# Kernel tuning notes

Measured on AMD Instinct MI355X. Metric: run time of the kernel, lower is better.

The kernel has to match this reference:

```python
import jax, jax.numpy as jnp
import numpy as np

N, G, NPG, K = 65536, 64, 1024, 32
NB, BD, IN_CH, GNN_DIM, L = 64, 4, 256, 256, 2
NBP = (BD - 1) * BD // 2 * NB  # 384
E = 524288


def setup_inputs():
    key = jax.random.key(0)
    ks = jax.random.split(key, 10)
    s = 0.05
    return {
        "x": jax.random.normal(ks[0], (N, IN_CH), jnp.float32),
        "eigvec": jax.random.normal(ks[1], (N, K), jnp.float32) / np.float32(np.sqrt(NPG)),
        "eigval": jax.random.uniform(ks[2], (G, K), jnp.float32, 0.0, 2.0),
        "taus": jnp.ones((NB,), jnp.float32),
        "enc_w": jax.random.normal(ks[3], (IN_CH, GNN_DIM), jnp.float32) * s,
        "enc_b": jnp.zeros((GNN_DIM,), jnp.float32),
        "self_w": jax.random.normal(ks[4], (L, GNN_DIM, GNN_DIM), jnp.float32) * s,
        "self_b": jnp.zeros((L, GNN_DIM), jnp.float32),
        "nb_w": jax.random.normal(ks[5], (L, GNN_DIM, GNN_DIM), jnp.float32) * s,
        "nb_b": jnp.zeros((L, GNN_DIM), jnp.float32),
        "dec_w": jax.random.normal(ks[6], (GNN_DIM, NBP), jnp.float32) * s,
        "dec_b": jnp.zeros((NBP,), jnp.float32),
        "lin_w": jax.random.normal(ks[7], (IN_CH, IN_CH), jnp.float32) * s,
        "lin_b": jnp.zeros((IN_CH,), jnp.float32),
        "edge_index": jax.random.randint(ks[8], (2, E), 0, N, jnp.int32),
    }


def _householder(p):
    # p: [M, BD*(BD-1)//2] -> Q: [M, BD, BD], product of BD-1 Householder reflectors
    M = p.shape[0]
    Q = jnp.broadcast_to(jnp.eye(BD, dtype=p.dtype), (M, BD, BD))
    idx = 0
    for j in range(BD - 1):  # small fixed loop over bundle_dim-1 reflectors
        n = BD - 1 - j
        v = jnp.zeros((M, BD), p.dtype).at[:, j].set(1.0)
        v = v.at[:, j + 1:].set(p[:, idx:idx + n])
        idx += n
        nrm = jnp.sum(v * v, axis=1)[:, None, None]
        Qv = jnp.einsum('mij,mj->mi', Q, v)
        Q = Q - 2.0 * Qv[:, :, None] * v[:, None, :] / nrm
    return Q


def reference(x, eigvec, eigval, taus, enc_w, enc_b, self_w, self_b,
              nb_w, nb_b, dec_w, dec_b, lin_w, lin_b, edge_index):
    gelu = lambda t: jax.nn.gelu(t, approximate=False)
    src, dst = edge_index[0], edge_index[1]
    vf = x.reshape(N, NB, BD, -1)                      # [N, NB, BD, 1]
    # SumGNN structural encoder: h = gelu(enc(x)); residual GNN layers; dec
    h = gelu(x @ enc_w + enc_b)
    for k in range(L):
        agg = jax.ops.segment_sum(h[src], dst, num_segments=N)  # sum aggregation
        hk = (h @ self_w[k] + self_b[k]) + (agg @ nb_w[k] + nb_b[k])
        h = gelu(hk) + h
    node_rep = h @ dec_w + dec_b                       # [N, NBP]
    Q = _householder(node_rep.reshape(N * NB, NBP // NB)).reshape(N, NB, BD, BD)
    vf = jnp.einsum('abcd,abde->abce', Q, vf)          # bundle transform
    h = vf.reshape(G, NPG, IN_CH)                      # to_dense_batch (equal-size graphs)
    ev = eigvec.reshape(G, NPG, K)
    hs = jnp.einsum('gnv,gnd->gvd', ev, h)             # project onto eigenbasis
    fact = jnp.exp(-eigval[:, :, None] * taus[None, None, :])   # [G, K, NB]
    hs = (hs.reshape(G, K, NB, BD, -1) * fact[..., None, None]).reshape(G, K, IN_CH)
    h = jnp.einsum('gnv,gvd->gnd', ev, hs).reshape(N, IN_CH)     # reproject
    h = h @ lin_w + lin_b
    vf = jnp.einsum('abdc,abde->abce', Q, h.reshape(N, NB, BD, -1))  # Q^T
    return vf.reshape(N, IN_CH)
```

## Files before the change

### kernel.cpp

```cpp
#include <hip/hip_runtime.h>
#include <math.h>

#define NN      65536
#define GG      64
#define NPG     1024
#define KEIG    32
#define NBUN    64
#define BDIM    4
#define CH      256
#define NBP     384
#define NEDGE   524288

using f16x8 = __attribute__((ext_vector_type(8))) _Float16;
using f16x4 = __attribute__((ext_vector_type(4))) _Float16;
using f32x4 = __attribute__((ext_vector_type(4))) float;

__device__ __forceinline__ float gelu_f(float x) {
    return 0.5f * x * (1.0f + erff(x * 0.70710678118654752440f));
}

template<int NOUT, int KTOT, bool DUAL, bool ACT, bool RESA, bool WF, bool W16>
__global__ __launch_bounds__(NOUT, 2) void mgemm_k(
    const _Float16* __restrict__ A1, const _Float16* __restrict__ A2,
    const _Float16* __restrict__ Bp, const float* __restrict__ bias,
    float* __restrict__ Cf, _Float16* __restrict__ C16)
{
    constexpr int NT   = KTOT / 32;
    constexpr int ROWB = KTOT * 2;
    constexpr int CPR  = KTOT / 8;
    __shared__ _Float16 Alds[64 * KTOT];

    const int tid  = threadIdx.x;
    const int lane = tid & 63;
    const int wave = tid >> 6;
    const int m0   = blockIdx.x * 64;

    constexpr int TOTC = 64 * CPR;
    constexpr int NSTG = TOTC / NOUT;
    {
        f16x8 stg[NSTG ? NSTG : 1];
#pragma unroll
        for (int j = 0; j < NSTG; j++) {
            const int idx = tid + j * NOUT;
            const int r = idx / CPR, c = idx - r * CPR;
            const _Float16* src = (DUAL && c >= CPR / 2)
                ? A2 + (size_t)(m0 + r) * 256 + (c - CPR / 2) * 8
                : A1 + (size_t)(m0 + r) * 256 + c * 8;
            stg[j] = *(const f16x8*)src;
        }
#pragma unroll
        for (int j = 0; j < NSTG; j++) {
            const int idx = tid + j * NOUT;
            const int r = idx / CPR, c = idx - r * CPR;
            *(f16x8*)((char*)Alds + ((r * ROWB + c * 16) ^ ((r & 7) << 4))) = stg[j];
        }
        if (TOTC % NOUT) {
            const int idx = tid + NSTG * NOUT;
            if (idx < TOTC) {
                const int r = idx / CPR, c = idx - r * CPR;
                const _Float16* src = (DUAL && c >= CPR / 2)
                    ? A2 + (size_t)(m0 + r) * 256 + (c - CPR / 2) * 8
                    : A1 + (size_t)(m0 + r) * 256 + c * 8;
                f16x8 v = *(const f16x8*)src;
                *(f16x8*)((char*)Alds + ((r * ROWB + c * 16) ^ ((r & 7) << 4))) = v;
            }
        }
    }
    __syncthreads();

    const int r16 = lane & 15;
    const int kc  = lane >> 4;

    const _Float16* bpp = Bp + ((size_t)wave * NT * 2048) + lane * 8;

    f32x4 acc[4][4];
#pragma unroll
    for (int i = 0; i < 4; i++)
#pragma unroll
        for (int j = 0; j < 4; j++) acc[i][j] = 0.f;

    f16x8 p00, p01, p02, p03, p10, p11, p12, p13;

#define LDB(P0, P1, P2, P3, T)                                                 \
    {                                                                          \
        const _Float16* bq_ = bpp + (size_t)(T) * 2048;                        \
        P0 = *(const f16x8*)(bq_);                                             \
        P1 = *(const f16x8*)(bq_ + 512);                                       \
        P2 = *(const f16x8*)(bq_ + 1024);                                      \
        P3 = *(const f16x8*)(bq_ + 1536);                                      \
    }

#define MSTEP(OFF, P0, P1, P2, P3)                                             \
    {                                                                          \
        const char* ap_ = (const char*)Alds + (OFF);                           \
        f16x8 a0_ = *(const f16x8*)(ap_);                                      \
        f16x8 a1_ = *(const f16x8*)(ap_ + 16 * ROWB);                          \
        f16x8 a2_ = *(const f16x8*)(ap_ + 32 * ROWB);                          \
        f16x8 a3_ = *(const f16x8*)(ap_ + 48 * ROWB);                          \
        acc[0][0] = __builtin_amdgcn_mfma_f32_16x16x32_f16(a0_, P0, acc[0][0], 0, 0, 0); \
        acc[0][1] = __builtin_amdgcn_mfma_f32_16x16x32_f16(a0_, P1, acc[0][1], 0, 0, 0); \
        acc[0][2] = __builtin_amdgcn_mfma_f32_16x16x32_f16(a0_, P2, acc[0][2], 0, 0, 0); \
        acc[0][3] = __builtin_amdgcn_mfma_f32_16x16x32_f16(a0_, P3, acc[0][3], 0, 0, 0); \
        acc[1][0] = __builtin_amdgcn_mfma_f32_16x16x32_f16(a1_, P0, acc[1][0], 0, 0, 0); \
        acc[1][1] = __builtin_amdgcn_mfma_f32_16x16x32_f16(a1_, P1, acc[1][1], 0, 0, 0); \
        acc[1][2] = __builtin_amdgcn_mfma_f32_16x16x32_f16(a1_, P2, acc[1][2], 0, 0, 0); \
        acc[1][3] = __builtin_amdgcn_mfma_f32_16x16x32_f16(a1_, P3, acc[1][3], 0, 0, 0); \
        acc[2][0] = __builtin_amdgcn_mfma_f32_16x16x32_f16(a2_, P0, acc[2][0], 0, 0, 0); \
        acc[2][1] = __builtin_amdgcn_mfma_f32_16x16x32_f16(a2_, P1, acc[2][1], 0, 0, 0); \
        acc[2][2] = __builtin_amdgcn_mfma_f32_16x16x32_f16(a2_, P2, acc[2][2], 0, 0, 0); \
        acc[2][3] = __builtin_amdgcn_mfma_f32_16x16x32_f16(a2_, P3, acc[2][3], 0, 0, 0); \
        acc[3][0] = __builtin_amdgcn_mfma_f32_16x16x32_f16(a3_, P0, acc[3][0], 0, 0, 0); \
        acc[3][1] = __builtin_amdgcn_mfma_f32_16x16x32_f16(a3_, P1, acc[3][1], 0, 0, 0); \
        acc[3][2] = __builtin_amdgcn_mfma_f32_16x16x32_f16(a3_, P2, acc[3][2], 0, 0, 0); \
        acc[3][3] = __builtin_amdgcn_mfma_f32_16x16x32_f16(a3_, P3, acc[3][3], 0, 0, 0); \
    }

    LDB(p00, p01, p02, p03, 0)
    LDB(p10, p11, p12, p13, 1)

    int au = r16 * ROWB + kc * 16;
    const int swz = (r16 & 7) << 4;
    for (int t = 0; t < NT; t += 2) {
        MSTEP(au ^ swz, p00, p01, p02, p03)
        if (t + 2 < NT) LDB(p00, p01, p02, p03, t + 2)
        MSTEP((au + 64) ^ swz, p10, p11, p12, p13)
        if (t + 3 < NT) LDB(p10, p11, p12, p13, t + 3)
        au += 128;
    }
#undef LDB
#undef MSTEP

    const int rbase = (lane >> 4) * 4;
    const int ncol  = lane & 15;
#pragma unroll
    for (int nt = 0; nt < 4; nt++) {
        const int n = wave * 64 + nt * 16 + ncol;
        const float bs = bias[n];
#pragma unroll
        for (int mt = 0; mt < 4; mt++) {
#pragma unroll
            for (int i = 0; i < 4; i++) {
                const int m = m0 + mt * 16 + rbase + i;
                const size_t idx = (size_t)m * NOUT + n;
                float v = acc[mt][nt][i] + bs;
                if (ACT) v = gelu_f(v);
                if (RESA) v += (float)A1[(size_t)m * 256 + n];
                if (WF) Cf[idx] = v;
                if (W16) C16[idx] = (_Float16)v;
            }
        }
    }
}

template<int NOUT, int KTOT, bool DUAL>
__global__ __launch_bounds__(256) void pack_k(
    const float* __restrict__ W1, const float* __restrict__ W2,
    _Float16* __restrict__ Bp)
{
    constexpr int NT = KTOT / 32;
    const int cid = blockIdx.x * 256 + threadIdx.x;
    if (cid >= NOUT * KTOT / 8) return;
    const int l  = cid & 63;
    const int q  = (cid >> 6) & 3;
    const int c2 = cid >> 8;
    const int t  = c2 & (NT - 1);
    const int wn = c2 / NT;
    const int n  = wn * 64 + q * 16 + (l & 15);
    const int k0 = t * 32 + (l >> 4) * 8;
    f16x8 v;
#pragma unroll
    for (int j = 0; j < 8; j++) {
        const int k = k0 + j;
        float w = (DUAL && k >= 256) ? W2[(size_t)(k - 256) * NOUT + n]
                                     : W1[(size_t)k * NOUT + n];
        v[j] = (_Float16)w;
    }
    *(f16x8*)(Bp + (size_t)cid * 8) = v;
}

__global__ void zero_k(float* __restrict__ p, size_t n)
{
    size_t i = (size_t)blockIdx.x * blockDim.x + threadIdx.x;
    float4* p4 = (float4*)p;
    size_t n4 = n >> 2;
    for (size_t j = i; j < n4; j += (size_t)gridDim.x * blockDim.x)
        p4[j] = make_float4(0.f, 0.f, 0.f, 0.f);
}

__global__ __launch_bounds__(256) void cvt16_k(
    const float* __restrict__ in, _Float16* __restrict__ out)
{
    size_t i = (size_t)blockIdx.x * 256 + threadIdx.x;
    float4 v = ((const float4*)in)[i];
    f16x4 o = { (_Float16)v.x, (_Float16)v.y, (_Float16)v.z, (_Float16)v.w };
    ((f16x4*)out)[i] = o;
}

__global__ void bcomb_k(const float* __restrict__ a, const float* __restrict__ b,
                        float* __restrict__ o)
{
    int i = blockIdx.x * 256 + threadIdx.x;
    if (i < 512) o[i] = a[i] + b[i];
}

__global__ __launch_bounds__(256) void hist_k(const int* __restrict__ ei, int* __restrict__ deg)
{
    int e = blockIdx.x * 256 + threadIdx.x;
    if (e < NEDGE) atomicAdd(&deg[ei[NEDGE + e]], 1);
}

__global__ __launch_bounds__(1024) void scan_k(
    const int* __restrict__ deg, int* __restrict__ off, int* __restrict__ cursor)
{
    __shared__ int sh[1024];
    const int tid = threadIdx.x;
    const int base = tid * 64;
    int s = 0;
#pragma unroll 8
    for (int i = 0; i < 64; i++) s += deg[base + i];
    const int mysum = s;
    sh[tid] = s;
    __syncthreads();
    for (int ofs = 1; ofs < 1024; ofs <<= 1) {
        int v = (tid >= ofs) ? sh[tid - ofs] : 0;
        __syncthreads();
        sh[tid] += v;
        __syncthreads();
    }
    int running = sh[tid] - mysum;
    for (int i = 0; i < 64; i++) {
        off[base + i] = running;
        cursor[base + i] = running;
        running += deg[base + i];
    }
    if (tid == 1023) off[NN] = running;
}

__global__ __launch_bounds__(256) void fill_k(
    const int* __restrict__ ei, int* __restrict__ cursor, int* __restrict__ csr)
{
    int e = blockIdx.x * 256 + threadIdx.x;
    if (e < NEDGE) {
        int d = ei[NEDGE + e];
        int pos = atomicAdd(&cursor[d], 1);
        csr[pos] = ei[e];
    }
}

__global__ __launch_bounds__(256) void gather16_k(
    const _Float16* __restrict__ h, const int* __restrict__ off,
    const int* __restrict__ csr, _Float16* __restrict__ agg)
{
    const int lane = threadIdx.x & 63;
    const int n = blockIdx.x * 4 + (threadIdx.x >> 6);
    const int s0 = off[n], s1 = off[n + 1];
    float a0 = 0.f, a1 = 0.f, a2 = 0.f, a3 = 0.f;
    int j = s0;
    for (; j + 1 < s1; j += 2) {
        f16x4 va = ((const f16x4*)(h + (size_t)csr[j] * CH))[lane];
        f16x4 vb = ((const f16x4*)(h + (size_t)csr[j + 1] * CH))[lane];
        a0 += (float)va[0] + (float)vb[0]; a1 += (float)va[1] + (float)vb[1];
        a2 += (float)va[2] + (float)vb[2]; a3 += (float)va[3] + (float)vb[3];
    }
    if (j < s1) {
        f16x4 va = ((const f16x4*)(h + (size_t)csr[j] * CH))[lane];
        a0 += (float)va[0]; a1 += (float)va[1]; a2 += (float)va[2]; a3 += (float)va[3];
    }
    f16x4 o = { (_Float16)a0, (_Float16)a1, (_Float16)a2, (_Float16)a3 };
    ((f16x4*)(agg + (size_t)n * CH))[lane] = o;
}

__device__ __forceinline__ void make_Q(const _Float16* __restrict__ p, float Q[4][4])
{
#pragma unroll
    for (int i = 0; i < 4; i++)
#pragma unroll
        for (int j = 0; j < 4; j++) Q[i][j] = (i == j) ? 1.f : 0.f;
    int idx = 0;
#pragma unroll
    for (int j = 0; j < 3; j++) {
        float v[4] = {0.f, 0.f, 0.f, 0.f};
        v[j] = 1.f;
#pragma unroll
        for (int t = 0; t < 4; t++)
            if (t > j) v[t] = (float)p[idx + t - (j + 1)];
        idx += 3 - j;
        float nrm = v[0]*v[0] + v[1]*v[1] + v[2]*v[2] + v[3]*v[3];
        float s = 2.f / nrm;
#pragma unroll
        for (int i = 0; i < 4; i++) {
            float qv = Q[i][0]*v[0] + Q[i][1]*v[1] + Q[i][2]*v[2] + Q[i][3]*v[3];
            float t0 = s * qv;
#pragma unroll
            for (int c = 0; c < 4; c++) Q[i][c] -= t0 * v[c];
        }
    }
}

template<bool TRANS>
__global__ __launch_bounds__(256) void bundle_k(
    const float* __restrict__ vin, const _Float16* __restrict__ nr,
    float* __restrict__ out)
{
    __shared__ _Float16 pb[4 * NBP];
    const int n0 = blockIdx.x * 4;
    for (int i = threadIdx.x; i < 4 * NBP; i += 256)
        pb[i] = nr[(size_t)n0 * NBP + i];
    __syncthreads();
    const int ln = threadIdx.x >> 6;
    const int b  = threadIdx.x & 63;
    const int n  = n0 + ln;
    float Q[4][4];
    make_Q(&pb[ln * NBP + b * 6], Q);
    float4 xv = ((const float4*)(vin + (size_t)n * CH))[b];
    float in0 = xv.x, in1 = xv.y, in2 = xv.z, in3 = xv.w;
    float4 o;
    if constexpr (!TRANS) {
        o.x = Q[0][0]*in0 + Q[0][1]*in1 + Q[0][2]*in2 + Q[0][3]*in3;
        o.y = Q[1][0]*in0 + Q[1][1]*in1 + Q[1][2]*in2 + Q[1][3]*in3;
        o.z = Q[2][0]*in0 + Q[2][1]*in1 + Q[2][2]*in2 + Q[2][3]*in3;
        o.w = Q[3][0]*in0 + Q[3][1]*in1 + Q[3][2]*in2 + Q[3][3]*in3;
    } else {
        o.x = Q[0][0]*in0 + Q[1][0]*in1 + Q[2][0]*in2 + Q[3][0]*in3;
        o.y = Q[0][1]*in0 + Q[1][1]*in1 + Q[2][1]*in2 + Q[3][1]*in3;
        o.z = Q[0][2]*in0 + Q[1][2]*in1 + Q[2][2]*in2 + Q[3][2]*in3;
        o.w = Q[0][3]*in0 + Q[1][3]*in1 + Q[2][3]*in2 + Q[3][3]*in3;
    }
    ((float4*)(out + (size_t)n * CH))[b] = o;
}

__global__ __launch_bounds__(256) void spec_proj_k(
    const float* __restrict__ v, const float* __restrict__ eigvec, float* __restrict__ hs)
{
    const int g = blockIdx.x;
    const int nbase = g * NPG + blockIdx.y * 128;
    __shared__ float evs[16][32];
    float acc[32];
#pragma unroll
    for (int k = 0; k < 32; k++) acc[k] = 0.f;
    for (int nt = 0; nt < 128; nt += 16) {
        __syncthreads();
        for (int i = threadIdx.x; i < 512; i += 256) {
            int nn = i >> 5, kk = i & 31;
            evs[nn][kk] = eigvec[(size_t)(nbase + nt + nn) * KEIG + kk];
        }
        __syncthreads();
#pragma unroll 4
        for (int nn = 0; nn < 16; nn++) {
            float hv = v[(size_t)(nbase + nt + nn) * CH + threadIdx.x];
#pragma unroll
            for (int k = 0; k < 32; k++) acc[k] += evs[nn][k] * hv;
        }
    }
    float* o = hs + (size_t)g * KEIG * CH + threadIdx.x;
#pragma unroll
    for (int k = 0; k < 32; k++) atomicAdd(o + k * CH, acc[k]);
}

__global__ __launch_bounds__(256) void spec_reproj16_k(
    const float* __restrict__ eigvec, const float* __restrict__ hs,
    const float* __restrict__ eigval, const float* __restrict__ taus,
    _Float16* __restrict__ out16)
{
    const int g = blockIdx.x >> 4;
    const int nbase = g * NPG + (blockIdx.x & 15) * 64;
    const float tau = taus[threadIdx.x >> 2];
    float hsr[32];
    const float* hg = hs + (size_t)g * KEIG * CH + threadIdx.x;
#pragma unroll
    for (int k = 0; k < 32; k++)
        hsr[k] = hg[k * CH] * expf(-eigval[g * KEIG + k] * tau);
    __shared__ float evs[64][32];
    for (int i = threadIdx.x; i < 2048; i += 256) {
        int nn = i >> 5, kk = i & 31;
        evs[nn][kk] = eigvec[(size_t)(nbase + nn) * KEIG + kk];
    }
    __syncthreads();
    for (int nn = 0; nn < 64; nn++) {
        float a = 0.f;
#pragma unroll
        for (int k = 0; k < 32; k++) a += evs[nn][k] * hsr[k];
        out16[(size_t)(nbase + nn) * CH + threadIdx.x] = (_Float16)a;
    }
}

extern "C" void kernel_launch(void* const* d_in, const int* in_sizes, int n_in,
                              void* d_out, int out_size, void* d_ws, size_t ws_size,
                              hipStream_t stream)
{
    const float* x      = (const float*)d_in[0];
    const float* eigvec = (const float*)d_in[1];
    const float* eigval = (const float*)d_in[2];
    const float* taus   = (const float*)d_in[3];
    const float* enc_w  = (const float*)d_in[4];
    const float* enc_b  = (const float*)d_in[5];
    const float* self_w = (const float*)d_in[6];
    const float* self_b = (const float*)d_in[7];
    const float* nb_w   = (const float*)d_in[8];
    const float* nb_b   = (const float*)d_in[9];
    const float* dec_w  = (const float*)d_in[10];
    const float* dec_b  = (const float*)d_in[11];
    const float* lin_w  = (const float*)d_in[12];
    const float* lin_b  = (const float*)d_in[13];
    const int*   ei     = (const int*)d_in[14];
    (void)in_sizes; (void)n_in; (void)out_size; (void)ws_size;

    float* ws = (float*)d_ws;
    _Float16* x16 = (_Float16*)(ws);
    _Float16* h0  = (_Float16*)(ws + 8388608);
    _Float16* h1  = (_Float16*)(ws + 16777216);
    _Float16* agg = (_Float16*)(ws + 25165824);
    int* ibase  = (int*)(ws + 33554432);
    int* deg    = ibase;
    int* off    = ibase + 65536;
    int* cursor = ibase + 131073;
    int* csr    = ibase + 196609;
    _Float16* nr16 = (_Float16*)(ws + 25165824);
    float* wb = ws + 37748752;
    _Float16* enc16 = (_Float16*)(wb);
    _Float16* l1w   = (_Float16*)(wb + 32768);
    _Float16* l2w   = (_Float16*)(wb + 98304);
    _Float16* dec16 = (_Float16*)(wb + 163840);
    _Float16* lin16 = (_Float16*)(wb + 212992);
    float* lbias = wb + 245760;
    _Float16* h2 = (_Float16*)(ws + 37995024);
    float* vf1 = ws;
    float* hs  = ws + 16777216;
    float* h3  = vf1;

    dim3 blk(256);

    cvt16_k<<<16384, blk, 0, stream>>>(x, x16);
    pack_k<256, 256, false><<<32, blk, 0, stream>>>(enc_w, nullptr, enc16);
    pack_k<256, 512, true ><<<64, blk, 0, stream>>>(self_w,         nb_w,         l1w);
    pack_k<256, 512, true ><<<64, blk, 0, stream>>>(self_w + 65536, nb_w + 65536, l2w);
    pack_k<384, 256, false><<<48, blk, 0, stream>>>(dec_w, nullptr, dec16);
    pack_k<256, 256, false><<<32, blk, 0, stream>>>(lin_w, nullptr, lin16);
    bcomb_k<<<2, blk, 0, stream>>>(self_b, nb_b, lbias);
    zero_k<<<64, blk, 0, stream>>>((float*)deg, (size_t)NN);
    hist_k<<<NEDGE / 256, blk, 0, stream>>>(ei, deg);
    scan_k<<<1, 1024, 0, stream>>>(deg, off, cursor);
    fill_k<<<NEDGE / 256, blk, 0, stream>>>(ei, cursor, csr);

    mgemm_k<256, 256, false, true, false, false, true><<<dim3(1024), blk, 0, stream>>>(
        x16, nullptr, enc16, enc_b, nullptr, h0);

    gather16_k<<<NN / 4, blk, 0, stream>>>(h0, off, csr, agg);
    mgemm_k<256, 512, true, true, true, false, true><<<dim3(1024), blk, 0, stream>>>(
        h0, agg, l1w, lbias, nullptr, h1);

    gather16_k<<<NN / 4, blk, 0, stream>>>(h1, off, csr, agg);
    mgemm_k<256, 512, true, true, true, false, true><<<dim3(1024), blk, 0, stream>>>(
        h1, agg, l2w, lbias + 256, nullptr, h0);

    mgemm_k<384, 256, false, false, false, false, true><<<dim3(1024), dim3(384), 0, stream>>>(
        h0, nullptr, dec16, dec_b, nullptr, nr16);

    bundle_k<false><<<NN / 4, blk, 0, stream>>>(x, nr16, vf1);

    zero_k<<<512, blk, 0, stream>>>(hs, (size_t)GG * KEIG * CH);
    spec_proj_k<<<dim3(GG, 8), blk, 0, stream>>>(vf1, eigvec, hs);
    spec_reproj16_k<<<GG * 16, blk, 0, stream>>>(eigvec, hs, eigval, taus, h2);

    mgemm_k<256, 256, false, false, false, true, false><<<dim3(1024), blk, 0, stream>>>(
        h2, nullptr, lin16, lin_b, h3, nullptr);

    bundle_k<true><<<NN / 4, blk, 0, stream>>>(h3, nr16, (float*)d_out);
}
```

Measured before the change: 711.5 us.

## Deepen B prefetch, stage fp16 epilogue through LDS, unroll gather by four

The GEMM kernel now issues B-fragment loads for four k-steps before the A tile is staged, so global B latency overlaps the LDS fill. The main loop uses a four-deep register ring and is fully unrolled. The fp16 output path writes results into a padded LDS tile and stores them as coalesced 16-byte rows instead of scattered 2-byte writes. The edge gather loop is unrolled by four to raise memory-level parallelism. In exchange, register pressure rises, which may lower occupancy under the launch bound of 2, and two extra barriers are added in the epilogue.

```diff
diff --git a/kernel.cpp b/kernel.cpp
--- a/kernel.cpp
+++ b/kernel.cpp
@@ -28,12 +28,38 @@
     constexpr int NT   = KTOT / 32;
     constexpr int ROWB = KTOT * 2;
     constexpr int CPR  = KTOT / 8;
-    __shared__ _Float16 Alds[64 * KTOT];
+    constexpr int CTS  = NOUT + 8;
+    constexpr int AH   = 64 * KTOT;
+    constexpr int CTH  = 64 * CTS;
+    constexpr int LDSH = (W16 && CTH > AH) ? CTH : AH;
+    __shared__ _Float16 Alds[LDSH];
 
     const int tid  = threadIdx.x;
     const int lane = tid & 63;
     const int wave = tid >> 6;
     const int m0   = blockIdx.x * 64;
+
+    const int r16 = lane & 15;
+    const int kc  = lane >> 4;
+
+    const _Float16* bpp = Bp + ((size_t)wave * NT * 2048) + lane * 8;
+
+    f16x8 pa0, pa1, pa2, pa3, pb0, pb1, pb2, pb3;
+    f16x8 pc0, pc1, pc2, pc3, pd0, pd1, pd2, pd3;
+
+#define LDB(P0, P1, P2, P3, T)                                                 \
+    {                                                                          \
+        const _Float16* bq_ = bpp + (size_t)(T) * 2048;                        \
+        P0 = *(const f16x8*)(bq_);                                             \
+        P1 = *(const f16x8*)(bq_ + 512);                                       \
+        P2 = *(const f16x8*)(bq_ + 1024);                                      \
+        P3 = *(const f16x8*)(bq_ + 1536);                                      \
+    }
+
+    LDB(pa0, pa1, pa2, pa3, 0)
+    LDB(pb0, pb1, pb2, pb3, 1)
+    LDB(pc0, pc1, pc2, pc3, 2)
+    LDB(pd0, pd1, pd2, pd3, 3)
 
     constexpr int TOTC = 64 * CPR;
     constexpr int NSTG = TOTC / NOUT;
@@ -68,27 +94,11 @@
     }
     __syncthreads();
 
-    const int r16 = lane & 15;
-    const int kc  = lane >> 4;
-
-    const _Float16* bpp = Bp + ((size_t)wave * NT * 2048) + lane * 8;
-
     f32x4 acc[4][4];
 #pragma unroll
     for (int i = 0; i < 4; i++)
 #pragma unroll
         for (int j = 0; j < 4; j++) acc[i][j] = 0.f;
-
-    f16x8 p00, p01, p02, p03, p10, p11, p12, p13;
-
-#define LDB(P0, P1, P2, P3, T)                                                 \
-    {                                                                          \
-        const _Float16* bq_ = bpp + (size_t)(T) * 2048;                        \
-        P0 = *(const f16x8*)(bq_);                                             \
-        P1 = *(const f16x8*)(bq_ + 512);                                       \
-        P2 = *(const f16x8*)(bq_ + 1024);                                      \
-        P3 = *(const f16x8*)(bq_ + 1536);                                      \
-    }
 
 #define MSTEP(OFF, P0, P1, P2, P3)                                             \
     {                                                                          \
@@ -115,38 +125,68 @@
         acc[3][3] = __builtin_amdgcn_mfma_f32_16x16x32_f16(a3_, P3, acc[3][3], 0, 0, 0); \
     }
 
-    LDB(p00, p01, p02, p03, 0)
-    LDB(p10, p11, p12, p13, 1)
-
     int au = r16 * ROWB + kc * 16;
     const int swz = (r16 & 7) << 4;
-    for (int t = 0; t < NT; t += 2) {
-        MSTEP(au ^ swz, p00, p01, p02, p03)
-        if (t + 2 < NT) LDB(p00, p01, p02, p03, t + 2)
-        MSTEP((au + 64) ^ swz, p10, p11, p12, p13)
-        if (t + 3 < NT) LDB(p10, p11, p12, p13, t + 3)
-        au += 128;
+#pragma unroll
+    for (int t = 0; t < NT; t += 4) {
+        MSTEP((au      ) ^ swz, pa0, pa1, pa2, pa3)
+        if (t + 4 < NT) LDB(pa0, pa1, pa2, pa3, t + 4)
+        MSTEP((au +  64) ^ swz, pb0, pb1, pb2, pb3)
+        if (t + 5 < NT) LDB(pb0, pb1, pb2, pb3, t + 5)
+        MSTEP((au + 128) ^ swz, pc0, pc1, pc2, pc3)
+        if (t + 6 < NT) LDB(pc0, pc1, pc2, pc3, t + 6)
+        MSTEP((au + 192) ^ swz, pd0, pd1, pd2, pd3)
+        if (t + 7 < NT) LDB(pd0, pd1, pd2, pd3, t + 7)
+        au += 256;
     }
 #undef LDB
 #undef MSTEP
 
     const int rbase = (lane >> 4) * 4;
     const int ncol  = lane & 15;
-#pragma unroll
-    for (int nt = 0; nt < 4; nt++) {
-        const int n = wave * 64 + nt * 16 + ncol;
-        const float bs = bias[n];
-#pragma unroll
-        for (int mt = 0; mt < 4; mt++) {
-#pragma unroll
-            for (int i = 0; i < 4; i++) {
-                const int m = m0 + mt * 16 + rbase + i;
-                const size_t idx = (size_t)m * NOUT + n;
-                float v = acc[mt][nt][i] + bs;
-                if (ACT) v = gelu_f(v);
-                if (RESA) v += (float)A1[(size_t)m * 256 + n];
-                if (WF) Cf[idx] = v;
-                if (W16) C16[idx] = (_Float16)v;
+    if constexpr (W16) {
+        __syncthreads();
+#pragma unroll
+        for (int nt = 0; nt < 4; nt++) {
+            const int n = wave * 64 + nt * 16 + ncol;
+            const float bs = bias[n];
+#pragma unroll
+            for (int mt = 0; mt < 4; mt++) {
+#pragma unroll
+                for (int i = 0; i < 4; i++) {
+                    const int mr = mt * 16 + rbase + i;
+                    float v = acc[mt][nt][i] + bs;
+                    if (ACT) v = gelu_f(v);
+                    if (RESA) v += (float)A1[(size_t)(m0 + mr) * 256 + n];
+                    Alds[mr * CTS + n] = (_Float16)v;
+                }
+            }
+        }
+        __syncthreads();
+        constexpr int CPRN = NOUT / 8;
+        constexpr int CPT  = 64 * CPRN / NOUT;
+#pragma unroll
+        for (int k2 = 0; k2 < CPT; k2++) {
+            const int c = tid + k2 * NOUT;
+            const int row = c / CPRN, col = c - row * CPRN;
+            f16x8 v = *(const f16x8*)&Alds[row * CTS + col * 8];
+            *(f16x8*)(C16 + (size_t)(m0 + row) * NOUT + col * 8) = v;
+        }
+    } else {
+#pragma unroll
+        for (int nt = 0; nt < 4; nt++) {
+            const int n = wave * 64 + nt * 16 + ncol;
+            const float bs = bias[n];
+#pragma unroll
+            for (int mt = 0; mt < 4; mt++) {
+#pragma unroll
+                for (int i = 0; i < 4; i++) {
+                    const int m = m0 + mt * 16 + rbase + i;
+                    float v = acc[mt][nt][i] + bs;
+                    if (ACT) v = gelu_f(v);
+                    if (RESA) v += (float)A1[(size_t)m * 256 + n];
+                    if (WF) Cf[(size_t)m * NOUT + n] = v;
+                }
             }
         }
     }
@@ -256,13 +296,18 @@
     const int s0 = off[n], s1 = off[n + 1];
     float a0 = 0.f, a1 = 0.f, a2 = 0.f, a3 = 0.f;
     int j = s0;
-    for (; j + 1 < s1; j += 2) {
-        f16x4 va = ((const f16x4*)(h + (size_t)csr[j] * CH))[lane];
-        f16x4 vb = ((const f16x4*)(h + (size_t)csr[j + 1] * CH))[lane];
-        a0 += (float)va[0] + (float)vb[0]; a1 += (float)va[1] + (float)vb[1];
-        a2 += (float)va[2] + (float)vb[2]; a3 += (float)va[3] + (float)vb[3];
-    }
-    if (j < s1) {
+    for (; j + 3 < s1; j += 4) {
+        const int i0 = csr[j], i1 = csr[j + 1], i2 = csr[j + 2], i3 = csr[j + 3];
+        f16x4 v0 = ((const f16x4*)(h + (size_t)i0 * CH))[lane];
+        f16x4 v1 = ((const f16x4*)(h + (size_t)i1 * CH))[lane];
+        f16x4 v2 = ((const f16x4*)(h + (size_t)i2 * CH))[lane];
+        f16x4 v3 = ((const f16x4*)(h + (size_t)i3 * CH))[lane];
+        a0 += (float)v0[0] + (float)v1[0] + (float)v2[0] + (float)v3[0];
+        a1 += (float)v0[1] + (float)v1[1] + (float)v2[1] + (float)v3[1];
+        a2 += (float)v0[2] + (float)v1[2] + (float)v2[2] + (float)v3[2];
+        a3 += (float)v0[3] + (float)v1[3] + (float)v2[3] + (float)v3[3];
+    }
+    for (; j < s1; j++) {
         f16x4 va = ((const f16x4*)(h + (size_t)csr[j] * CH))[lane];
         a0 += (float)va[0]; a1 += (float)va[1]; a2 += (float)va[2]; a3 += (float)va[3];
     }
```

Result: faster. 694.2 us (-2.4%).
